# Kernel tuning notes

Measured on AMD Instinct MI355X. Metric: run time of the kernel, lower is better.

The kernel has to match this reference:

```python
import jax, jax.numpy as jnp
import numpy as np

EPS = 1e-5

def _layer_norm(x, w, b):
    mu = jnp.mean(x, axis=-1, keepdims=True)
    var = jnp.mean(jnp.square(x - mu), axis=-1, keepdims=True)
    return (x - mu) * jax.lax.rsqrt(var + EPS) * w + b

def setup_inputs() -> dict:
    key = jax.random.key(0)
    ks = jax.random.split(key, 4)
    B, S, H, D = 8, 2048, 8, 64
    E = H * D  # hidden_size = 512
    x = jax.random.normal(ks[0], (B * S, E), dtype=jnp.float32)
    w_uvqk = jax.random.normal(ks[1], (E, 4 * H * D), dtype=jnp.float32) * (E ** -0.5)
    b_uvqk = jax.random.normal(ks[2], (4 * H * D,), dtype=jnp.float32) * 0.02
    w_proj = jax.random.normal(ks[3], (H * D, E), dtype=jnp.float32) * ((H * D) ** -0.5)
    return {
        "x": x,
        "w_uvqk": w_uvqk,
        "b_uvqk": b_uvqk,
        "ln_in_w": jnp.ones((E,), jnp.float32),
        "ln_in_b": jnp.zeros((E,), jnp.float32),
        "ln_out_w": jnp.ones((H * D,), jnp.float32),
        "ln_out_b": jnp.zeros((H * D,), jnp.float32),
        "w_proj": w_proj,
        "batch_size": B,
        "max_seqlen": S,
        "num_targets": 64,
    }

def reference(x, w_uvqk, b_uvqk, ln_in_w, ln_in_b, ln_out_w, ln_out_b, w_proj,
              batch_size, max_seqlen, num_targets):
    B, S = batch_size, max_seqlen
    E = x.shape[-1]
    HD = w_proj.shape[0]          # num_heads * head_dim
    D = 64
    H = HD // D
    alpha = 1.0 / (D ** 0.5)

    # input layer norm
    xn = _layer_norm(x, ln_in_w, ln_in_b)                      # [T, E]
    # fused addmm + silu -> u, v, q, k
    mixed = jax.nn.silu(xn @ w_uvqk + b_uvqk)                  # [T, 4*H*D]
    u, v, q, k = jnp.split(mixed, 4, axis=-1)
    q = q.reshape(B, S, H, D)
    k = k.reshape(B, S, H, D)
    v = v.reshape(B, S, H, D)

    # HSTU silu attention: attn = silu(alpha * q k^T) / scaling_seqlen, masked
    scores = jnp.einsum("bshd,bthd->bhst", q, k) * alpha       # [B,H,S,S]
    attn = jax.nn.silu(scores) / jnp.float32(S)

    # causal mask + target mask: targets (last num_targets positions) are keys
    # only for themselves (target_group_size = 1)
    i = jnp.arange(S)[:, None]
    j = jnp.arange(S)[None, :]
    causal = j <= i
    key_is_history = j < (S - num_targets)
    mask = causal & (key_is_history | (i == j))                # [S,S]
    attn = jnp.where(mask[None, None], attn, 0.0)

    attn_out = jnp.einsum("bhst,bthd->bshd", attn, v)          # [B,S,H,D]
    attn_out = attn_out.reshape(B * S, HD)

    # ln_mul: u * layer_norm(attn_out)
    parallel = u * _layer_norm(attn_out, ln_out_w, ln_out_b)   # [T, HD]

    # residual projection
    out = parallel @ w_proj + x                                # [T, E]
    return out
```

## Files before the change

kernel.cpp:

```cpp
#include <hip/hip_runtime.h>
#include <hip/hip_bf16.h>

#define Bc 8
#define Sc 2048
#define Hc 8
#define Dc 64
#define Ec 512
#define NTc 64
#define Tc (Bc*Sc)
#define N1c (4*Hc*Dc)
#define HISTc (Sc - NTc)

typedef float f32x4 __attribute__((ext_vector_type(4)));
typedef __bf16 bf16x8 __attribute__((ext_vector_type(8)));
typedef short short8 __attribute__((ext_vector_type(8)));
typedef short s4v __attribute__((ext_vector_type(4)));

__device__ __forceinline__ unsigned short f2bf(float f){
  unsigned int u = __float_as_uint(f);
  u += 0x7fffu + ((u >> 16) & 1u);
  return (unsigned short)(u >> 16);
}
__device__ __forceinline__ float bf2f(unsigned short h){
  return __uint_as_float(((unsigned int)h) << 16);
}
__device__ __forceinline__ unsigned int pkbf(float a, float b){
  float2 f; f.x = a; f.y = b;
  __hip_bfloat162 h = __float22bfloat162_rn(f);
  unsigned int u;
  __builtin_memcpy(&u, &h, 4);
  return u;
}
__device__ __forceinline__ s4v pk4(float a, float b, float c, float d){
  uint2 u; u.x = pkbf(a, b); u.y = pkbf(c, d);
  return __builtin_bit_cast(s4v, u);
}
__device__ __forceinline__ float silu_f(float x){
  return x * __builtin_amdgcn_rcpf(1.f + __expf(-x));
}
__device__ __forceinline__ bf16x8 ldb8(const unsigned short* p){
  return __builtin_bit_cast(bf16x8, *(const short8*)p);
}
__device__ __forceinline__ f32x4 mfma16(bf16x8 a, bf16x8 b, f32x4 c){
  return __builtin_amdgcn_mfma_f32_16x16x32_bf16(a, b, c, 0, 0, 0);
}
__device__ __forceinline__ void gl_lds16(const void* g, void* l){
  __builtin_amdgcn_global_load_lds((const __attribute__((address_space(1))) unsigned int*)g,
                                   (__attribute__((address_space(3))) unsigned int*)l, 16, 0, 0);
}

__global__ __launch_bounds__(1024) void k_transpose_cast(const float* __restrict__ in,
                                                         unsigned short* __restrict__ out,
                                                         int R, int C){
  __shared__ float tile[32][33];
  int tx = threadIdx.x, ty = threadIdx.y;
  int c0 = blockIdx.x * 32, r0 = blockIdx.y * 32;
  tile[ty][tx] = in[(size_t)(r0 + ty) * C + c0 + tx];
  __syncthreads();
  out[(size_t)(c0 + ty) * R + r0 + tx] = f2bf(tile[tx][ty]);
}

__global__ __launch_bounds__(256) void k_ln_in(const float* __restrict__ x, const float* __restrict__ g,
                                               const float* __restrict__ b, unsigned short* __restrict__ xn){
  int lane = threadIdx.x & 63;
  int row = blockIdx.x * 4 + (threadIdx.x >> 6);
  const float* xr = x + (size_t)row * Ec + lane * 8;
  float4 v0 = *(const float4*)xr;
  float4 v1 = *(const float4*)(xr + 4);
  float vv[8] = {v0.x, v0.y, v0.z, v0.w, v1.x, v1.y, v1.z, v1.w};
  float s = 0.f, ss = 0.f;
  #pragma unroll
  for (int j = 0; j < 8; ++j){ s += vv[j]; ss += vv[j] * vv[j]; }
  #pragma unroll
  for (int m = 1; m < 64; m <<= 1){ s += __shfl_xor(s, m); ss += __shfl_xor(ss, m); }
  float mu = s * (1.f / Ec);
  float rs = rsqrtf(ss * (1.f / Ec) - mu * mu + 1e-5f);
  int c = lane * 8;
  float o[8];
  #pragma unroll
  for (int j = 0; j < 8; ++j) o[j] = (vv[j] - mu) * rs * g[c + j] + b[c + j];
  uint4 pk; pk.x = pkbf(o[0], o[1]); pk.y = pkbf(o[2], o[3]);
  pk.z = pkbf(o[4], o[5]); pk.w = pkbf(o[6], o[7]);
  *(uint4*)(xn + (size_t)row * Ec + c) = pk;
}

__global__ __launch_bounds__(256) void k_ln_mul(const unsigned short* __restrict__ att, const float* __restrict__ g,
                                                const float* __restrict__ b, const unsigned short* __restrict__ u,
                                                unsigned short* __restrict__ par){
  int lane = threadIdx.x & 63;
  int row = blockIdx.x * 4 + (threadIdx.x >> 6);
  short8 a8 = *(const short8*)(att + (size_t)row * Ec + lane * 8);
  short8 u8 = *(const short8*)(u + (size_t)row * Ec + lane * 8);
  float vv[8];
  #pragma unroll
  for (int j = 0; j < 8; ++j) vv[j] = bf2f((unsigned short)a8[j]);
  float s = 0.f, ss = 0.f;
  #pragma unroll
  for (int j = 0; j < 8; ++j){ s += vv[j]; ss += vv[j] * vv[j]; }
  #pragma unroll
  for (int m = 1; m < 64; m <<= 1){ s += __shfl_xor(s, m); ss += __shfl_xor(ss, m); }
  float mu = s * (1.f / Ec);
  float rs = rsqrtf(ss * (1.f / Ec) - mu * mu + 1e-5f);
  int c = lane * 8;
  float o[8];
  #pragma unroll
  for (int j = 0; j < 8; ++j){
    float uu = bf2f((unsigned short)u8[j]);
    o[j] = uu * ((vv[j] - mu) * rs * g[c + j] + b[c + j]);
  }
  uint4 pk; pk.x = pkbf(o[0], o[1]); pk.y = pkbf(o[2], o[3]);
  pk.z = pkbf(o[4], o[5]); pk.w = pkbf(o[6], o[7]);
  *(uint4*)(par + (size_t)row * Ec + c) = pk;
}

__global__ __launch_bounds__(256) void k_gemm_uvqk(const unsigned short* __restrict__ A,
                                                   const unsigned short* __restrict__ BT,
                                                   const float* __restrict__ bias,
                                                   unsigned short* __restrict__ u_out,
                                                   unsigned short* __restrict__ vT,
                                                   unsigned short* __restrict__ qb,
                                                   unsigned short* __restrict__ kb){
  __shared__ __align__(16) unsigned short As[2][128 * 32];
  __shared__ __align__(16) unsigned short Bs[2][128 * 32];
  int tid = threadIdx.x;
  int lane = tid & 63, w = tid >> 6;
  int lm = lane & 15, quad = lane >> 4;
  int wm = w & 1, wn = w >> 1;
  int bid = blockIdx.y * gridDim.x + blockIdx.x;
  int id2 = (bid & 7) * 256 + (bid >> 3);
  int n0 = (id2 & 15) << 7, m0 = (id2 >> 4) << 7;
  int cat = n0 >> 9;
  bool swp = (cat != 1);
  int xc = quad ^ ((lm >> 1) & 3);

  int r0s = tid >> 2, c0s = ((tid & 3) ^ ((r0s >> 1) & 3)) * 16;
  int r1s = r0s + 64;
  const char* saA0 = (const char*)(A  + (size_t)(m0 + r0s) * Ec) + c0s;
  const char* saA1 = (const char*)(A  + (size_t)(m0 + r1s) * Ec) + c0s;
  const char* saB0 = (const char*)(BT + (size_t)(n0 + r0s) * Ec) + c0s;
  const char* saB1 = (const char*)(BT + (size_t)(n0 + r1s) * Ec) + c0s;

  gl_lds16(saA0, (char*)As[0] + tid * 16);
  gl_lds16(saA1, (char*)As[0] + tid * 16 + 4096);
  gl_lds16(saB0, (char*)Bs[0] + tid * 16);
  gl_lds16(saB1, (char*)Bs[0] + tid * 16 + 4096);
  __syncthreads();

  f32x4 acc[4][4] = {};
  #pragma unroll 1
  for (int kt = 0; kt < 16; ++kt){
    int cur = kt & 1, nb = cur ^ 1;
    if (kt < 15){
      int k0 = (kt + 1) * 64;
      gl_lds16(saA0 + k0, (char*)As[nb] + tid * 16);
      gl_lds16(saA1 + k0, (char*)As[nb] + tid * 16 + 4096);
      gl_lds16(saB0 + k0, (char*)Bs[nb] + tid * 16);
      gl_lds16(saB1 + k0, (char*)Bs[nb] + tid * 16 + 4096);
    }
    bf16x8 af[4], bfr[4];
    #pragma unroll
    for (int s = 0; s < 4; ++s)
      af[s]  = ldb8(As[cur] + ((wm * 64 + s * 16 + lm) * 4 + xc) * 8);
    #pragma unroll
    for (int t = 0; t < 4; ++t)
      bfr[t] = ldb8(Bs[cur] + ((wn * 64 + t * 16 + lm) * 4 + xc) * 8);
    if (swp){
      #pragma unroll
      for (int s = 0; s < 4; ++s)
        #pragma unroll
        for (int t = 0; t < 4; ++t)
          acc[s][t] = mfma16(bfr[t], af[s], acc[s][t]);
    } else {
      #pragma unroll
      for (int s = 0; s < 4; ++s)
        #pragma unroll
        for (int t = 0; t < 4; ++t)
          acc[s][t] = mfma16(af[s], bfr[t], acc[s][t]);
    }
    __syncthreads();
  }

  if (cat == 1){
    #pragma unroll
    for (int t = 0; t < 4; ++t){
      int colg = n0 + wn * 64 + t * 16 + lm;
      float bv = bias[colg];
      int c = colg & 511, h = c >> 6, d = c & 63;
      #pragma unroll
      for (int s = 0; s < 4; ++s){
        int row = m0 + wm * 64 + s * 16 + quad * 4;
        int bb_ = row >> 11, sr = row & (Sc - 1);
        s4v pv = pk4(silu_f(acc[s][t][0] + bv), silu_f(acc[s][t][1] + bv),
                     silu_f(acc[s][t][2] + bv), silu_f(acc[s][t][3] + bv));
        *(s4v*)(vT + ((size_t)(bb_ * Hc + h) * Dc + d) * Sc + sr) = pv;
      }
    }
  } else {
    #pragma unroll
    for (int s = 0; s < 4; ++s){
      int row = m0 + wm * 64 + s * 16 + lm;
      int bb_ = row >> 11, sr = row & (Sc - 1);
      #pragma unroll
      for (int t = 0; t < 4; ++t){
        int colg = n0 + wn * 64 + t * 16 + quad * 4;
        float4 bv = *(const float4*)(bias + colg);
        float v0 = silu_f(acc[s][t][0] + bv.x);
        float v1 = silu_f(acc[s][t][1] + bv.y);
        float v2 = silu_f(acc[s][t][2] + bv.z);
        float v3 = silu_f(acc[s][t][3] + bv.w);
        int c = colg & 511, h = c >> 6, d = c & 63;
        if (cat == 0){
          *(s4v*)(u_out + (size_t)row * Ec + c) = pk4(v0, v1, v2, v3);
        } else if (cat == 2){
          *(s4v*)(qb + ((size_t)(bb_ * Hc + h) * Sc + sr) * Dc + d) =
            pk4(v0 * 0.125f, v1 * 0.125f, v2 * 0.125f, v3 * 0.125f);
        } else {
          *(s4v*)(kb + ((size_t)(bb_ * Hc + h) * Sc + sr) * Dc + d) = pk4(v0, v1, v2, v3);
        }
      }
    }
  }
}

__global__ __launch_bounds__(256) void k_attn(const unsigned short* __restrict__ qb,
                                              const unsigned short* __restrict__ kb,
                                              const unsigned short* __restrict__ vT,
                                              unsigned short* __restrict__ att){
  __shared__ __align__(16) unsigned short Kb[2][64 * 64];
  __shared__ __align__(16) unsigned short Vb[2][64 * 64];
  int tid = threadIdx.x;
  int lane = tid & 63, w = tid >> 6;
  int lm = lane & 15, quad = lane >> 4;
  int lmx = lm & 7;
  int bid = blockIdx.y * gridDim.x + blockIdx.x;
  int id2 = (bid & 7) * 256 + (bid >> 3);
  int bh = id2 >> 5;
  int qblk = 31 - (id2 & 31);
  int qrow = qblk * 64 + w * 16;
  int lastT = qblk;
  int ntiles = lastT + 1;

  const unsigned short* kbp = kb + (size_t)bh * Sc * Dc;
  const unsigned short* vbp = vT + (size_t)bh * Dc * Sc;
  const unsigned short* qp = qb + ((size_t)bh * Sc + qrow + lm) * Dc + quad * 8;
  bf16x8 qa0 = ldb8(qp), qa1 = ldb8(qp + 32);

  int r0s = tid >> 3, c0s = ((tid & 7) ^ (r0s & 7)) * 16;
  int r1s = (tid + 256) >> 3, c1s = (((tid + 256) & 7) ^ (r1s & 7)) * 16;
  const char* kS0 = (const char*)kbp + (size_t)r0s * 128 + c0s;
  const char* kS1 = (const char*)kbp + (size_t)r1s * 128 + c1s;
  const char* vS0 = (const char*)vbp + (size_t)r0s * (Sc * 2) + c0s;
  const char* vS1 = (const char*)vbp + (size_t)r1s * (Sc * 2) + c1s;

  {
    gl_lds16(kS0, (char*)Kb[0] + tid * 16);
    gl_lds16(kS1, (char*)Kb[0] + tid * 16 + 4096);
    gl_lds16(vS0, (char*)Vb[0] + tid * 16);
    gl_lds16(vS1, (char*)Vb[0] + tid * 16 + 4096);
  }
  __syncthreads();

  f32x4 o[4] = {};
  int qg = qrow + lm;
  for (int kt = 0; kt < ntiles; ++kt){
    int cur = kt & 1, nb = cur ^ 1;
    if (kt + 1 < ntiles){
      int knb = (kt + 1) * 128;
      gl_lds16(kS0 + (size_t)(kt + 1) * 8192, (char*)Kb[nb] + tid * 16);
      gl_lds16(kS1 + (size_t)(kt + 1) * 8192, (char*)Kb[nb] + tid * 16 + 4096);
      gl_lds16(vS0 + knb, (char*)Vb[nb] + tid * 16);
      gl_lds16(vS1 + knb, (char*)Vb[nb] + tid * 16 + 4096);
    }
    const unsigned short* Kc = Kb[cur];
    const unsigned short* Vc = Vb[cur];
    bool maskT = (kt == lastT);
    int key0 = kt * 64;
    #pragma unroll
    for (int s = 0; s < 4; ++s){
      int krow = (s * 16 + lm) * 8;
      bf16x8 kf0 = ldb8(Kc + (krow + (quad ^ lmx)) * 8);
      bf16x8 kf1 = ldb8(Kc + (krow + ((quad + 4) ^ lmx)) * 8);
      f32x4 sc = {0.f, 0.f, 0.f, 0.f};
      sc = mfma16(kf0, qa0, sc);
      sc = mfma16(kf1, qa1, sc);
      s4v pf;
      if (maskT){
        float m[4];
        #pragma unroll
        for (int r = 0; r < 4; ++r){
          int kg = key0 + s * 16 + quad * 4 + r;
          bool ok = (kg <= qg) && ((kg < HISTc) || (kg == qg));
          m[r] = ok ? silu_f(sc[r]) : 0.f;
        }
        pf = pk4(m[0], m[1], m[2], m[3]);
      } else {
        pf = pk4(silu_f(sc[0]), silu_f(sc[1]), silu_f(sc[2]), silu_f(sc[3]));
      }
      #pragma unroll
      for (int t = 0; t < 4; ++t){
        int vrow = (t * 16 + lm) * 8;
        s4v vf = *(const s4v*)(Vc + (vrow + ((2 * s + (quad >> 1)) ^ lmx)) * 8 + (quad & 1) * 4);
        o[t] = __builtin_amdgcn_mfma_f32_16x16x16bf16_1k(pf, vf, o[t], 0, 0, 0);
      }
    }
    __syncthreads();
  }
  int bb_ = bh >> 3, hh = bh & 7;
  #pragma unroll
  for (int t = 0; t < 4; ++t){
    int d = t * 16 + lm;
    unsigned int p01 = pkbf(o[t][0] * (1.f / Sc), o[t][1] * (1.f / Sc));
    unsigned int p23 = pkbf(o[t][2] * (1.f / Sc), o[t][3] * (1.f / Sc));
    size_t base = ((size_t)(bb_ * Sc + qrow + quad * 4) * Hc + hh) * Dc + d;
    att[base]               = (unsigned short)p01;
    att[base + Hc * Dc]     = (unsigned short)(p01 >> 16);
    att[base + 2 * Hc * Dc] = (unsigned short)p23;
    att[base + 3 * Hc * Dc] = (unsigned short)(p23 >> 16);
  }
}

__global__ __launch_bounds__(256) void k_gemm_proj(const unsigned short* __restrict__ A,
                                                   const unsigned short* __restrict__ BT,
                                                   const float* __restrict__ x,
                                                   float* __restrict__ out){
  __shared__ __align__(16) unsigned short As[2][128 * 32];
  __shared__ __align__(16) unsigned short Bs[2][128 * 32];
  int tid = threadIdx.x;
  int lane = tid & 63, w = tid >> 6;
  int lm = lane & 15, quad = lane >> 4;
  int wm = w & 1, wn = w >> 1;
  int bid = blockIdx.y * gridDim.x + blockIdx.x;
  int id2 = (bid & 7) * 64 + (bid >> 3);
  int n0 = (id2 & 3) << 7, m0 = (id2 >> 2) << 7;
  int xc = quad ^ ((lm >> 1) & 3);

  int r0s = tid >> 2, c0s = ((tid & 3) ^ ((r0s >> 1) & 3)) * 16;
  int r1s = r0s + 64;
  const char* saA0 = (const char*)(A  + (size_t)(m0 + r0s) * Ec) + c0s;
  const char* saA1 = (const char*)(A  + (size_t)(m0 + r1s) * Ec) + c0s;
  const char* saB0 = (const char*)(BT + (size_t)(n0 + r0s) * Ec) + c0s;
  const char* saB1 = (const char*)(BT + (size_t)(n0 + r1s) * Ec) + c0s;

  gl_lds16(saA0, (char*)As[0] + tid * 16);
  gl_lds16(saA1, (char*)As[0] + tid * 16 + 4096);
  gl_lds16(saB0, (char*)Bs[0] + tid * 16);
  gl_lds16(saB1, (char*)Bs[0] + tid * 16 + 4096);
  __syncthreads();

  f32x4 acc[4][4] = {};
  #pragma unroll 1
  for (int kt = 0; kt < 16; ++kt){
    int cur = kt & 1, nb = cur ^ 1;
    if (kt < 15){
      int k0 = (kt + 1) * 64;
      gl_lds16(saA0 + k0, (char*)As[nb] + tid * 16);
      gl_lds16(saA1 + k0, (char*)As[nb] + tid * 16 + 4096);
      gl_lds16(saB0 + k0, (char*)Bs[nb] + tid * 16);
      gl_lds16(saB1 + k0, (char*)Bs[nb] + tid * 16 + 4096);
    }
    bf16x8 af[4], bfr[4];
    #pragma unroll
    for (int s = 0; s < 4; ++s)
      af[s]  = ldb8(As[cur] + ((wm * 64 + s * 16 + lm) * 4 + xc) * 8);
    #pragma unroll
    for (int t = 0; t < 4; ++t)
      bfr[t] = ldb8(Bs[cur] + ((wn * 64 + t * 16 + lm) * 4 + xc) * 8);
    #pragma unroll
    for (int s = 0; s < 4; ++s)
      #pragma unroll
      for (int t = 0; t < 4; ++t)
        acc[s][t] = mfma16(bfr[t], af[s], acc[s][t]);
    __syncthreads();
  }

  #pragma unroll
  for (int s = 0; s < 4; ++s){
    int row = m0 + wm * 64 + s * 16 + lm;
    #pragma unroll
    for (int t = 0; t < 4; ++t){
      int col = n0 + wn * 64 + t * 16 + quad * 4;
      float4 xr = *(const float4*)(x + (size_t)row * Ec + col);
      float4 o4 = {acc[s][t][0] + xr.x, acc[s][t][1] + xr.y,
                   acc[s][t][2] + xr.z, acc[s][t][3] + xr.w};
      *(float4*)(out + (size_t)row * Ec + col) = o4;
    }
  }
}

extern "C" void kernel_launch(void* const* d_in, const int* in_sizes, int n_in,
                              void* d_out, int out_size, void* d_ws, size_t ws_size,
                              hipStream_t stream){
  (void)in_sizes; (void)n_in; (void)out_size; (void)ws_size;
  const float* x        = (const float*)d_in[0];
  const float* w_uvqk   = (const float*)d_in[1];
  const float* b_uvqk   = (const float*)d_in[2];
  const float* ln_in_w  = (const float*)d_in[3];
  const float* ln_in_b  = (const float*)d_in[4];
  const float* ln_out_w = (const float*)d_in[5];
  const float* ln_out_b = (const float*)d_in[6];
  const float* w_proj   = (const float*)d_in[7];
  float* out = (float*)d_out;

  char* ws = (char*)d_ws;
  unsigned short* xn  = (unsigned short*)(ws + 0);
  unsigned short* wuT = (unsigned short*)(ws + 16777216);
  unsigned short* wpT = (unsigned short*)(ws + 18874368);
  unsigned short* ub  = (unsigned short*)(ws + 19398656);
  unsigned short* qbf = (unsigned short*)(ws + 52953088);
  unsigned short* kbf = (unsigned short*)(ws + 69730304);
  unsigned short* vTt = (unsigned short*)(ws + 86507520);
  unsigned short* att = (unsigned short*)(ws + 103284736);

  dim3 tb(32, 32);
  k_transpose_cast<<<dim3(N1c / 32, Ec / 32), tb, 0, stream>>>(w_uvqk, wuT, Ec, N1c);
  k_transpose_cast<<<dim3(Ec / 32, Ec / 32), tb, 0, stream>>>(w_proj, wpT, Ec, Ec);
  k_ln_in<<<Tc / 4, 256, 0, stream>>>(x, ln_in_w, ln_in_b, xn);
  k_gemm_uvqk<<<dim3(N1c / 128, Tc / 128), 256, 0, stream>>>(xn, wuT, b_uvqk, ub, vTt, qbf, kbf);
  k_attn<<<dim3(Bc * Hc, Sc / 64), 256, 0, stream>>>(qbf, kbf, vTt, att);
  k_ln_mul<<<Tc / 4, 256, 0, stream>>>(att, ln_out_w, ln_out_b, ub, xn);
  k_gemm_proj<<<dim3(Ec / 128, Tc / 128), 256, 0, stream>>>(xn, wpT, x, out);
}
```

Before: 293.5 us.

## Use 16x16x32 MFMA for PV via permlane16 swap and unroll double-buffer loop

The attention inner loop now packs the silu probabilities into bf16 pairs and uses v_permlane16_swap to rearrange them into the A-operand layout of the 16x16x32 MFMA. This halves the number of PV MFMA instructions and lets V fragments load as 16-byte vectors instead of 8-byte ones. The K-tile loop is unrolled by two with fixed buffer pointers, which removes the runtime cur/next indexing, and s_setprio raises priority around the PV MFMA block. The V LDS offsets are recomputed for the new layout, so the result depends on the permlane swap producing exactly the operand ordering that the MFMA expects.

New measurement: 285.9 us. 1.03x faster.

```diff
diff --git a/kernel.cpp b/kernel.cpp
--- a/kernel.cpp
+++ b/kernel.cpp
@@ -47,6 +47,9 @@
 __device__ __forceinline__ void gl_lds16(const void* g, void* l){
   __builtin_amdgcn_global_load_lds((const __attribute__((address_space(1))) unsigned int*)g,
                                    (__attribute__((address_space(3))) unsigned int*)l, 16, 0, 0);
+}
+__device__ __forceinline__ void pswap16(unsigned int &a, unsigned int &b){
+  asm volatile("v_permlane16_swap_b32 %0, %1" : "+v"(a), "+v"(b));
 }
 
 __global__ __launch_bounds__(1024) void k_transpose_cast(const float* __restrict__ in,
@@ -262,49 +265,73 @@
 
   f32x4 o[4] = {};
   int qg = qrow + lm;
-  for (int kt = 0; kt < ntiles; ++kt){
-    int cur = kt & 1, nb = cur ^ 1;
-    if (kt + 1 < ntiles){
-      int knb = (kt + 1) * 128;
-      gl_lds16(kS0 + (size_t)(kt + 1) * 8192, (char*)Kb[nb] + tid * 16);
-      gl_lds16(kS1 + (size_t)(kt + 1) * 8192, (char*)Kb[nb] + tid * 16 + 4096);
-      gl_lds16(vS0 + knb, (char*)Vb[nb] + tid * 16);
-      gl_lds16(vS1 + knb, (char*)Vb[nb] + tid * 16 + 4096);
-    }
-    const unsigned short* Kc = Kb[cur];
-    const unsigned short* Vc = Vb[cur];
+  int g = ((quad & 1) << 1) | (quad >> 1);
+  int koff0 = lm * 64 + (quad ^ lmx) * 8;
+  int koff1 = lm * 64 + (((quad + 4)) ^ lmx) * 8;
+  int voff0 = lm * 64 + ((g ^ lmx)) * 8;
+  int voff1 = lm * 64 + (((g + 4) ^ lmx)) * 8;
+
+  auto step = [&](const unsigned short* Kc, const unsigned short* Vc,
+                  char* dK, char* dV, int kt, bool do_stage){
+    if (do_stage){
+      gl_lds16(kS0 + (size_t)(kt + 1) * 8192, dK);
+      gl_lds16(kS1 + (size_t)(kt + 1) * 8192, dK + 4096);
+      gl_lds16(vS0 + (size_t)(kt + 1) * 128, dV);
+      gl_lds16(vS1 + (size_t)(kt + 1) * 128, dV + 4096);
+    }
     bool maskT = (kt == lastT);
     int key0 = kt * 64;
+    unsigned int dlo[4], dhi[4];
     #pragma unroll
     for (int s = 0; s < 4; ++s){
-      int krow = (s * 16 + lm) * 8;
-      bf16x8 kf0 = ldb8(Kc + (krow + (quad ^ lmx)) * 8);
-      bf16x8 kf1 = ldb8(Kc + (krow + ((quad + 4) ^ lmx)) * 8);
+      bf16x8 kf0 = ldb8(Kc + koff0 + s * 1024);
+      bf16x8 kf1 = ldb8(Kc + koff1 + s * 1024);
       f32x4 sc = {0.f, 0.f, 0.f, 0.f};
       sc = mfma16(kf0, qa0, sc);
       sc = mfma16(kf1, qa1, sc);
-      s4v pf;
+      float p[4];
       if (maskT){
-        float m[4];
         #pragma unroll
         for (int r = 0; r < 4; ++r){
           int kg = key0 + s * 16 + quad * 4 + r;
           bool ok = (kg <= qg) && ((kg < HISTc) || (kg == qg));
-          m[r] = ok ? silu_f(sc[r]) : 0.f;
+          p[r] = ok ? silu_f(sc[r]) : 0.f;
         }
-        pf = pk4(m[0], m[1], m[2], m[3]);
       } else {
-        pf = pk4(silu_f(sc[0]), silu_f(sc[1]), silu_f(sc[2]), silu_f(sc[3]));
+        #pragma unroll
+        for (int r = 0; r < 4; ++r) p[r] = silu_f(sc[r]);
       }
-      #pragma unroll
-      for (int t = 0; t < 4; ++t){
-        int vrow = (t * 16 + lm) * 8;
-        s4v vf = *(const s4v*)(Vc + (vrow + ((2 * s + (quad >> 1)) ^ lmx)) * 8 + (quad & 1) * 4);
-        o[t] = __builtin_amdgcn_mfma_f32_16x16x16bf16_1k(pf, vf, o[t], 0, 0, 0);
-      }
-    }
+      dlo[s] = pkbf(p[0], p[1]);
+      dhi[s] = pkbf(p[2], p[3]);
+    }
+    pswap16(dlo[0], dlo[1]); pswap16(dhi[0], dhi[1]);
+    pswap16(dlo[2], dlo[3]); pswap16(dhi[2], dhi[3]);
+    uint4 pa0u, pa1u;
+    pa0u.x = dlo[0]; pa0u.y = dhi[0]; pa0u.z = dlo[1]; pa0u.w = dhi[1];
+    pa1u.x = dlo[2]; pa1u.y = dhi[2]; pa1u.z = dlo[3]; pa1u.w = dhi[3];
+    bf16x8 pa0 = __builtin_bit_cast(bf16x8, pa0u);
+    bf16x8 pa1 = __builtin_bit_cast(bf16x8, pa1u);
+    __builtin_amdgcn_s_setprio(1);
+    #pragma unroll
+    for (int t = 0; t < 4; ++t){
+      bf16x8 vf0 = ldb8(Vc + voff0 + t * 1024);
+      bf16x8 vf1 = ldb8(Vc + voff1 + t * 1024);
+      o[t] = mfma16(pa0, vf0, o[t]);
+      o[t] = mfma16(pa1, vf1, o[t]);
+    }
+    __builtin_amdgcn_s_setprio(0);
     __syncthreads();
-  }
+  };
+
+  int kt = 0;
+  #pragma unroll 1
+  for (; kt + 2 <= ntiles; kt += 2){
+    step(Kb[0], Vb[0], (char*)Kb[1] + tid * 16, (char*)Vb[1] + tid * 16, kt, true);
+    step(Kb[1], Vb[1], (char*)Kb[0] + tid * 16, (char*)Vb[0] + tid * 16, kt + 1, kt + 2 < ntiles);
+  }
+  if (kt < ntiles)
+    step(Kb[0], Vb[0], (char*)Kb[1] + tid * 16, (char*)Vb[1] + tid * 16, kt, false);
+
   int bb_ = bh >> 3, hh = bh & 7;
   #pragma unroll
   for (int t = 0; t < 4; ++t){
```
